# Kernel optimization log

Measured on AMD Instinct MI355X. Metric: run time of the kernel, lower is better.

## Reference

```python
import jax, jax.numpy as jnp
import numpy as np

B, L, HID = 4, 1024, 1024
H, D = 16, 64  # num heads, head size


def setup_inputs() -> dict:
    key = jax.random.key(0)
    ks = jax.random.split(key, 12)
    s = 0.02
    return {
        "hidden_states": jax.random.normal(ks[0], (B, L, HID), jnp.float32),
        "attention_mask": jnp.zeros((B, 1, 1, L), jnp.float32),
        "structure_matrix": jax.random.normal(ks[1], (L, L, D), jnp.float32),
        # torch nn.Linear weights are [out, in]
        "Wq": jax.random.normal(ks[2], (H * D, HID), jnp.float32) * s,
        "bq": jnp.zeros((H * D,), jnp.float32),
        "Wk": jax.random.normal(ks[3], (H * D, HID), jnp.float32) * s,
        "bk": jnp.zeros((H * D,), jnp.float32),
        "Wv": jax.random.normal(ks[4], (H * D, HID), jnp.float32) * s,
        "bv": jnp.zeros((H * D,), jnp.float32),
        "Wsq": jax.random.normal(ks[5], (D, D), jnp.float32) * s,
        "bsq": jnp.zeros((D,), jnp.float32),
        "Wsk": jax.random.normal(ks[6], (D, D), jnp.float32) * s,
        "bsk": jnp.zeros((D,), jnp.float32),
    }


def _heads(x):
    # [B, L, H*D] -> [B, H, L, D]
    return x.reshape(B, L, H, D).transpose(0, 2, 1, 3)


def reference(hidden_states, attention_mask, structure_matrix,
              Wq, bq, Wk, bk, Wv, bv, Wsq, bsq, Wsk, bsk):
    q = _heads(hidden_states @ Wq.T + bq)  # [B,H,L,D]
    k = _heads(hidden_states @ Wk.T + bk)
    v = _heads(hidden_states @ Wv.T + bv)

    scores = jnp.einsum('bhld,bhrd->bhlr', q, k)

    sq = structure_matrix @ Wsq.T + bsq  # [L,L,D]
    sk = structure_matrix @ Wsk.T + bsk
    scores = scores + jnp.einsum('bhld,lrd->bhlr', q, sq) \
                    + jnp.einsum('bhrd,lrd->bhlr', k, sk)

    scores = scores / jnp.sqrt(jnp.float32(D)) + attention_mask
    probs = jax.nn.softmax(scores, axis=-1)
    ctx = jnp.einsum('bhlr,bhrd->bhld', probs, v)
    ctx = ctx.transpose(0, 2, 1, 3).reshape(B, L, H * D)
    return ctx, scores
```

## Files before the change

kernel.cpp:

```cpp
#include <hip/hip_runtime.h>

typedef __attribute__((ext_vector_type(8))) short short8v;
typedef __attribute__((ext_vector_type(4))) short short4v;
typedef __attribute__((ext_vector_type(4))) float float4v;
typedef __attribute__((ext_vector_type(2))) unsigned int uint2v;

#define MFMA16(a,b,c) __builtin_amdgcn_mfma_f32_16x16x32_bf16(a,b,c,0,0,0)

__device__ __forceinline__ unsigned short f2b(float f) {
    union { float f; unsigned u; } v; v.f = f;
    unsigned r = v.u + 0x7FFFu + ((v.u >> 16) & 1u);
    return (unsigned short)(r >> 16);
}
__device__ __forceinline__ float b2f(unsigned short s) {
    union { unsigned u; float f; } v; v.u = ((unsigned)s) << 16;
    return v.f;
}
__device__ __forceinline__ short8v pack8(float4v a, float4v b) {
    union { unsigned u[4]; short8v s; } o;
    asm("v_cvt_pk_bf16_f32 %0, %1, %2" : "=v"(o.u[0]) : "v"(a[0]), "v"(a[1]));
    asm("v_cvt_pk_bf16_f32 %0, %1, %2" : "=v"(o.u[1]) : "v"(a[2]), "v"(a[3]));
    asm("v_cvt_pk_bf16_f32 %0, %1, %2" : "=v"(o.u[2]) : "v"(b[0]), "v"(b[1]));
    asm("v_cvt_pk_bf16_f32 %0, %1, %2" : "=v"(o.u[3]) : "v"(b[2]), "v"(b[3]));
    return o.s;
}

__global__ __launch_bounds__(256) void pack_all(
    const float* __restrict__ hidden, const float* __restrict__ Wq,
    const float* __restrict__ Wk, const float* __restrict__ Wv,
    unsigned short* __restrict__ hb, unsigned short* __restrict__ Wqb,
    unsigned short* __restrict__ Wkb, unsigned short* __restrict__ Wvb) {
    const int bid = blockIdx.x;
    const float* in; unsigned short* out; int i;
    if (bid < 2048)      { in = hidden; out = hb;  i = bid * 256 + threadIdx.x; }
    else if (bid < 2560) { in = Wq; out = Wqb; i = (bid - 2048) * 256 + threadIdx.x; }
    else if (bid < 3072) { in = Wk; out = Wkb; i = (bid - 2560) * 256 + threadIdx.x; }
    else                 { in = Wv; out = Wvb; i = (bid - 3072) * 256 + threadIdx.x; }
    float4v a = *(const float4v*)&in[(size_t)i * 8];
    float4v b = *(const float4v*)&in[(size_t)i * 8 + 4];
    *(short8v*)&out[(size_t)i * 8] = pack8(a, b);
}

__global__ __launch_bounds__(256) void qkv_gemm(
    const unsigned short* __restrict__ A,
    const unsigned short* __restrict__ W,
    const float* __restrict__ bias,
    unsigned short* __restrict__ out, int vmode) {
    const int wave = threadIdx.x >> 6, lane = threadIdx.x & 63;
    const int m0 = blockIdx.y * 128 + wave * 32;
    const int n0 = blockIdx.x * 64;
    const int lrow = lane & 15, g8 = (lane >> 4) << 3, row4 = (lane >> 4) << 2;
    float4v acc[2][4] = {};
    const unsigned short* Ap = A + (size_t)(m0 + lrow) * 1024 + g8;
    const unsigned short* Wp = W + (size_t)(n0 + lrow) * 1024 + g8;
#pragma unroll 2
    for (int k0 = 0; k0 < 1024; k0 += 32) {
        short8v a0 = *(const short8v*)(Ap + k0);
        short8v a1 = *(const short8v*)(Ap + 16 * 1024 + k0);
        short8v b0 = *(const short8v*)(Wp + k0);
        short8v b1 = *(const short8v*)(Wp + 16 * 1024 + k0);
        short8v b2 = *(const short8v*)(Wp + 32 * 1024 + k0);
        short8v b3 = *(const short8v*)(Wp + 48 * 1024 + k0);
        acc[0][0] = MFMA16(a0, b0, acc[0][0]); acc[0][1] = MFMA16(a0, b1, acc[0][1]);
        acc[0][2] = MFMA16(a0, b2, acc[0][2]); acc[0][3] = MFMA16(a0, b3, acc[0][3]);
        acc[1][0] = MFMA16(a1, b0, acc[1][0]); acc[1][1] = MFMA16(a1, b1, acc[1][1]);
        acc[1][2] = MFMA16(a1, b2, acc[1][2]); acc[1][3] = MFMA16(a1, b3, acc[1][3]);
    }
#pragma unroll
    for (int nt = 0; nt < 4; ++nt) {
        const int n = n0 + nt * 16 + lrow;
        const float bz = bias[n];
        const int h = n >> 6, d = n & 63;
#pragma unroll
        for (int mt = 0; mt < 2; ++mt) {
            const int mb = m0 + mt * 16 + row4;
            if (vmode == 0) {
#pragma unroll
                for (int j = 0; j < 4; ++j) {
                    const int m = mb + j;
                    const int b = m >> 10, l = m & 1023;
                    out[(((size_t)(b * 16 + h) << 10) + l) * 64 + d] = f2b(acc[mt][nt][j] + bz);
                }
            } else {
                const int b = mb >> 10, r = mb & 1023;
                short4v pk;
#pragma unroll
                for (int j = 0; j < 4; ++j) pk[j] = (short)f2b(acc[mt][nt][j] + bz);
                *(short4v*)&out[((((size_t)(b * 16 + h)) << 6) + d) * 1024 + r] = pk;
            }
        }
    }
}

__global__ __launch_bounds__(256) void headproj(
    const unsigned short* __restrict__ xh,
    const float* __restrict__ Wsx,
    const float* __restrict__ bsx,
    unsigned short* __restrict__ x2b,
    float* __restrict__ xbv) {
    __shared__ __align__(16) float Ws[64 * 64];
    __shared__ float bs[64];
    __shared__ __align__(16) unsigned short Xl[64 * 64];
    const int tid = threadIdx.x;
    const int l = blockIdx.x;
#pragma unroll
    for (int i = 0; i < 4; ++i)
        *(float4v*)&Ws[tid * 4 + i * 1024] = *(const float4v*)&Wsx[tid * 4 + i * 1024];
    if (tid < 64) bs[tid] = bsx[tid];
    {
        const int bhh = tid >> 2, dq = (tid & 3) * 16;
        const unsigned short* src = &xh[((size_t)bhh * 1024 + l) * 64 + dq];
        *(short8v*)&Xl[bhh * 64 + dq] = *(const short8v*)src;
        *(short8v*)&Xl[bhh * 64 + dq + 8] = *(const short8v*)(src + 8);
    }
    __syncthreads();
    const int bh = tid >> 2, e0 = (tid & 3) * 16;
    float acc[16] = {};
    float bacc = 0.f;
    for (int d = 0; d < 64; ++d) {
        const float xd = b2f(Xl[bh * 64 + d]);
        bacc += xd * bs[d];
        const float* wr = &Ws[d * 64 + e0];
#pragma unroll
        for (int e = 0; e < 16; e += 4) {
            float4v w = *(const float4v*)&wr[e];
            acc[e] += xd * w[0]; acc[e + 1] += xd * w[1];
            acc[e + 2] += xd * w[2]; acc[e + 3] += xd * w[3];
        }
    }
    short8v p0, p1;
#pragma unroll
    for (int e = 0; e < 8; ++e) { p0[e] = (short)f2b(acc[e]); p1[e] = (short)f2b(acc[e + 8]); }
    unsigned short* dst = &x2b[((size_t)l * 64 + bh) * 64 + e0];
    *(short8v*)dst = p0; *(short8v*)(dst + 8) = p1;
    if ((tid & 3) == 0) xbv[l * 64 + bh] = bacc;
}

__global__ __launch_bounds__(256, 4) void struct_fused(
    const float* __restrict__ S,
    const unsigned short* __restrict__ q2b,
    const unsigned short* __restrict__ k2b,
    const float* __restrict__ qbv,
    const float* __restrict__ kbv,
    unsigned short* __restrict__ sb) {
    __shared__ __align__(16) unsigned short Ssh[256 * 64];
    __shared__ __align__(16) unsigned short t3g[4][4][16][16];
    const int tid = threadIdx.x;
    const int w = tid >> 6, lane = tid & 63;
    const int lrow = lane & 15, g = lane >> 4;
    const int g8 = g << 3, row4 = g << 2;
    const int w16 = w << 4;
    const int r0 = blockIdx.x << 4, l0 = blockIdx.y << 4;

    {
        const int u = tid & 15, roff = tid >> 4;
        const float* gp = S + ((size_t)l0 * 1024 + r0 + roff) * 64 + u * 4;
        float4v f[16];
#pragma unroll
        for (int i = 0; i < 16; ++i)
            f[i] = *(const float4v*)(gp + (size_t)i * 65536);
#pragma unroll
        for (int i = 0; i < 16; ++i) {
            const int R = (i << 4) + roff;
            const int K3 = (roff ^ i) & 7;
            const int pu = u ^ (K3 << 1);
            union { unsigned uu[2]; uint2v v2; } o;
            asm("v_cvt_pk_bf16_f32 %0, %1, %2" : "=v"(o.uu[0]) : "v"(f[i][0]), "v"(f[i][1]));
            asm("v_cvt_pk_bf16_f32 %0, %1, %2" : "=v"(o.uu[1]) : "v"(f[i][2]), "v"(f[i][3]));
            *(uint2v*)&Ssh[(R << 6) + (pu << 2)] = o.v2;
        }
    }
    float kbreg[4];
#pragma unroll
    for (int j = 0; j < 4; ++j)
        kbreg[j] = kbv[(size_t)(r0 + row4 + j) * 64 + w16 + lrow];
    __syncthreads();

    float4v c3[16];
#pragma unroll
    for (int ri = 0; ri < 16; ++ri) {
        const int row = lrow * 16 + ri;
        const int key = (lrow ^ ri) & 7;
        short8v a0 = *(const short8v*)&Ssh[row * 64 + ((g ^ key) << 3)];
        short8v a1 = *(const short8v*)&Ssh[row * 64 + (((4 + g) ^ key) << 3)];
        const unsigned short* Bp = k2b + ((size_t)(r0 + ri) * 64 + w16 + lrow) * 64 + g8;
        short8v b0 = *(const short8v*)Bp;
        short8v b1 = *(const short8v*)(Bp + 32);
        float4v acc = {};
        acc = MFMA16(a0, b0, acc);
        acc = MFMA16(a1, b1, acc);
        c3[ri] = acc;
    }

#pragma unroll
    for (int G = 0; G < 4; ++G) {
        if (g == G) {
#pragma unroll
            for (int j = 0; j < 4; ++j) {
                float4v la{c3[0][j], c3[1][j], c3[2][j], c3[3][j]};
                float4v lb{c3[4][j], c3[5][j], c3[6][j], c3[7][j]};
                float4v ha{c3[8][j], c3[9][j], c3[10][j], c3[11][j]};
                float4v hb{c3[12][j], c3[13][j], c3[14][j], c3[15][j]};
                *(short8v*)&t3g[w][j][lrow][0] = pack8(la, lb);
                *(short8v*)&t3g[w][j][lrow][8] = pack8(ha, hb);
            }
        }
        asm volatile("s_waitcnt lgkmcnt(0)" ::: "memory");
#pragma unroll
        for (int lj = 0; lj < 4; ++lj) {
            const int li = (G << 2) + lj;
            const int row = li * 16 + lrow;
            const int key = (li ^ lrow) & 7;
            short8v a0 = *(const short8v*)&Ssh[row * 64 + ((g ^ key) << 3)];
            short8v a1 = *(const short8v*)&Ssh[row * 64 + (((4 + g) ^ key) << 3)];
            const unsigned short* Bp = q2b + ((size_t)(l0 + li) * 64 + w16 + lrow) * 64 + g8;
            short8v b0 = *(const short8v*)Bp;
            short8v b1 = *(const short8v*)(Bp + 32);
            float4v c2 = {};
            c2 = MFMA16(a0, b0, c2);
            c2 = MFMA16(a1, b1, c2);
            short4v t3v = *(const short4v*)&t3g[w][lj][lrow][row4];
            const float qb = qbv[(size_t)(l0 + li) * 64 + w16 + lrow];
            short4v outv;
#pragma unroll
            for (int j = 0; j < 4; ++j)
                outv[j] = (short)f2b(c2[j] + b2f((unsigned short)t3v[j]) + qb + kbreg[j]);
            *(short4v*)&sb[((size_t)(l0 + li) * 64 + w16 + lrow) * 1024 + r0 + row4] = outv;
        }
    }
}

__global__ __launch_bounds__(256) void flash_kernel(
    const unsigned short* __restrict__ qh,
    const unsigned short* __restrict__ kh,
    const unsigned short* __restrict__ vT,
    const unsigned short* __restrict__ sb,
    const float* __restrict__ mask,
    float* __restrict__ scores,
    float* __restrict__ ctx) {
    __shared__ __align__(16) float scL[32 * 64];
    __shared__ __align__(16) unsigned short pL[32 * 64];
    __shared__ float mL[32], sL[32], fL[32];
    const int bid = blockIdx.x;
    const int virt = (bid & 7) * 256 + (bid >> 3);
    const int bh = virt >> 5, lt = virt & 31;
    const int b = bh >> 4, h = bh & 15, l0 = lt * 32;
    const int tid = threadIdx.x, wave = tid >> 6, lane = tid & 63;
    const int lrow = lane & 15, g8 = (lane >> 4) << 3, row4 = (lane >> 4) << 2;
    short8v qf[2][2];
#pragma unroll
    for (int mt = 0; mt < 2; ++mt)
#pragma unroll
        for (int ks = 0; ks < 2; ++ks)
            qf[mt][ks] = *(const short8v*)&qh[((size_t)bh * 1024 + l0 + mt * 16 + lrow) * 64 + ks * 32 + g8];
    float4v opv[2] = {};
    if (tid < 32) { mL[tid] = -3e38f; sL[tid] = 0.f; }
    __syncthreads();
    const int tl = tid >> 3, tr8 = tid & 7;
    const int keyS = ((tl >> 2) & 3) << 4;
    const int keyP = (tl & 7) << 3;
    for (int rt = 0; rt < 16; ++rt) {
        const int r0 = rt * 64;
        float4v sacc[2] = {};
#pragma unroll
        for (int ks = 0; ks < 2; ++ks) {
            short8v kf = *(const short8v*)&kh[((size_t)bh * 1024 + r0 + wave * 16 + lrow) * 64 + ks * 32 + g8];
            sacc[0] = MFMA16(qf[0][ks], kf, sacc[0]);
            sacc[1] = MFMA16(qf[1][ks], kf, sacc[1]);
        }
#pragma unroll
        for (int mt = 0; mt < 2; ++mt)
#pragma unroll
            for (int j = 0; j < 4; ++j) {
                const int ll = mt * 16 + row4 + j;
                const int cc = wave * 16 + lrow;
                scL[ll * 64 + (cc ^ (((ll >> 2) & 3) << 4))] = sacc[mt][j];
            }
        __syncthreads();
        float4v x0 = *(const float4v*)&scL[tl * 64 + ((tr8 * 8) ^ keyS)];
        float4v x1 = *(const float4v*)&scL[tl * 64 + ((tr8 * 8 + 4) ^ keyS)];
        short8v sbv = *(const short8v*)&sb[((size_t)(l0 + tl) * 64 + bh) * 1024 + r0 + tr8 * 8];
        float4v mk0 = *(const float4v*)&mask[(size_t)b * 1024 + r0 + tr8 * 8];
        float4v mk1 = *(const float4v*)&mask[(size_t)b * 1024 + r0 + tr8 * 8 + 4];
        float s8[8];
#pragma unroll
        for (int i = 0; i < 4; ++i) {
            s8[i]     = (x0[i] + b2f((unsigned short)sbv[i])) * 0.125f + mk0[i];
            s8[i + 4] = (x1[i] + b2f((unsigned short)sbv[i + 4])) * 0.125f + mk1[i];
        }
        {
            float4v o0, o1;
#pragma unroll
            for (int i = 0; i < 4; ++i) { o0[i] = s8[i]; o1[i] = s8[i + 4]; }
            float* sgp = &scores[((size_t)bh * 1024 + l0 + tl) * 1024 + r0 + tr8 * 8];
            *(float4v*)sgp = o0; *(float4v*)(sgp + 4) = o1;
        }
        float tm = s8[0];
#pragma unroll
        for (int i = 1; i < 8; ++i) tm = fmaxf(tm, s8[i]);
        tm = fmaxf(tm, __shfl_xor(tm, 1));
        tm = fmaxf(tm, __shfl_xor(tm, 2));
        tm = fmaxf(tm, __shfl_xor(tm, 4));
        const float mold = mL[tl];
        const float mnew = fmaxf(mold, tm);
        const float f = __expf(mold - mnew);
        float psum = 0.f;
        float p8[8];
#pragma unroll
        for (int i = 0; i < 8; ++i) { p8[i] = __expf(s8[i] - mnew); psum += p8[i]; }
        psum += __shfl_xor(psum, 1);
        psum += __shfl_xor(psum, 2);
        psum += __shfl_xor(psum, 4);
        if (tr8 == 0) { sL[tl] = sL[tl] * f + psum; mL[tl] = mnew; fL[tl] = f; }
        short8v pk;
#pragma unroll
        for (int i = 0; i < 8; ++i) pk[i] = (short)f2b(p8[i]);
        *(short8v*)&pL[tl * 64 + ((tr8 * 8) ^ keyP)] = pk;
        __syncthreads();
#pragma unroll
        for (int mt = 0; mt < 2; ++mt)
#pragma unroll
            for (int j = 0; j < 4; ++j) opv[mt][j] *= fL[mt * 16 + row4 + j];
#pragma unroll
        for (int ks = 0; ks < 2; ++ks) {
            short8v pf0 = *(const short8v*)&pL[(lrow) * 64 + ((ks * 32 + g8) ^ ((lrow & 7) << 3))];
            short8v pf1 = *(const short8v*)&pL[(16 + lrow) * 64 + ((ks * 32 + g8) ^ ((lrow & 7) << 3))];
            short8v vf = *(const short8v*)&vT[((size_t)bh * 64 + wave * 16 + lrow) * 1024 + r0 + ks * 32 + g8];
            opv[0] = MFMA16(pf0, vf, opv[0]);
            opv[1] = MFMA16(pf1, vf, opv[1]);
        }
    }
#pragma unroll
    for (int mt = 0; mt < 2; ++mt)
#pragma unroll
        for (int j = 0; j < 4; ++j) {
            const int l = mt * 16 + row4 + j;
            const float inv = 1.f / sL[l];
            const int d = wave * 16 + lrow;
            ctx[((size_t)b * 1024 + l0 + l) * 1024 + h * 64 + d] = opv[mt][j] * inv;
        }
}

extern "C" void kernel_launch(void* const* d_in, const int* in_sizes, int n_in,
                              void* d_out, int out_size, void* d_ws, size_t ws_size,
                              hipStream_t stream) {
    (void)in_sizes; (void)n_in; (void)out_size; (void)ws_size;
    const float* hidden = (const float*)d_in[0];
    const float* mask   = (const float*)d_in[1];
    const float* S      = (const float*)d_in[2];
    const float* Wq  = (const float*)d_in[3];  const float* bq  = (const float*)d_in[4];
    const float* Wk  = (const float*)d_in[5];  const float* bk  = (const float*)d_in[6];
    const float* Wv  = (const float*)d_in[7];  const float* bv  = (const float*)d_in[8];
    const float* Wsq = (const float*)d_in[9];  const float* bsq = (const float*)d_in[10];
    const float* Wsk = (const float*)d_in[11]; const float* bsk = (const float*)d_in[12];

    float* ctx    = (float*)d_out;
    float* scores = ctx + (size_t)4 * 1024 * 1024;

    char* ws = (char*)d_ws;
    unsigned short* sbuf = (unsigned short*)ws;
    unsigned short* hb  = (unsigned short*)ws;
    unsigned short* Wqb = (unsigned short*)(ws + (8u << 20));
    unsigned short* Wkb = (unsigned short*)(ws + (10u << 20));
    unsigned short* Wvb = (unsigned short*)(ws + (12u << 20));
    unsigned short* qh  = (unsigned short*)(ws + (size_t)(128u) * 1024 * 1024);
    unsigned short* kh  = qh  + (size_t)4 * 1024 * 1024;
    unsigned short* vT  = kh  + (size_t)4 * 1024 * 1024;
    unsigned short* q2b = vT  + (size_t)4 * 1024 * 1024;
    unsigned short* k2b = q2b + (size_t)4 * 1024 * 1024;
    float* qbv = (float*)(k2b + (size_t)4 * 1024 * 1024);
    float* kbv = qbv + 65536;

    pack_all<<<3584, 256, 0, stream>>>(hidden, Wq, Wk, Wv, hb, Wqb, Wkb, Wvb);
    qkv_gemm<<<dim3(16, 32), 256, 0, stream>>>(hb, Wqb, bq, qh, 0);
    qkv_gemm<<<dim3(16, 32), 256, 0, stream>>>(hb, Wkb, bk, kh, 0);
    qkv_gemm<<<dim3(16, 32), 256, 0, stream>>>(hb, Wvb, bv, vT, 1);
    headproj<<<1024, 256, 0, stream>>>(qh, Wsq, bsq, q2b, qbv);
    headproj<<<1024, 256, 0, stream>>>(kh, Wsk, bsk, k2b, kbv);
    struct_fused<<<dim3(64, 64), 256, 0, stream>>>(S, q2b, k2b, qbv, kbv, sbuf);
    flash_kernel<<<2048, 256, 0, stream>>>(qh, kh, vT, sbuf, mask, scores, ctx);
}
```

Baseline: 541.7 us.

## Give each wave its own query rows in flash kernel and merge QKV GEMM launches

The flash kernel now assigns each wave an independent 32-row query tile, so a block covers 128 rows and the grid drops to 512 blocks. Each wave computes transposed score tiles (K as the A operand), keeps row max and sum in registers with cross-lane shuffles, and stages P in a per-wave double-buffered LDS slot. This removes the block-wide __syncthreads and the shared-memory score round trip. The three QKV GEMM launches are merged into one 48-column grid that picks Q, K or V weights by block index. In exchange, each wave reloads its own K and V tiles and holds more accumulator registers, and fewer blocks are launched.

```diff
diff --git a/kernel.cpp b/kernel.cpp
--- a/kernel.cpp
+++ b/kernel.cpp
@@ -43,12 +43,20 @@
 
 __global__ __launch_bounds__(256) void qkv_gemm(
     const unsigned short* __restrict__ A,
-    const unsigned short* __restrict__ W,
-    const float* __restrict__ bias,
-    unsigned short* __restrict__ out, int vmode) {
+    const unsigned short* __restrict__ Wqb, const unsigned short* __restrict__ Wkb,
+    const unsigned short* __restrict__ Wvb,
+    const float* __restrict__ bq, const float* __restrict__ bk,
+    const float* __restrict__ bv,
+    unsigned short* __restrict__ outq) {
+    const int n0g = blockIdx.x * 64;
+    const int which = n0g >> 10;
+    const int n0 = n0g & 1023;
+    const unsigned short* W = (which == 0) ? Wqb : (which == 1) ? Wkb : Wvb;
+    const float* bias = (which == 0) ? bq : (which == 1) ? bk : bv;
+    unsigned short* out = outq + (size_t)which * 4194304;
+    const int vmode = (which == 2);
     const int wave = threadIdx.x >> 6, lane = threadIdx.x & 63;
     const int m0 = blockIdx.y * 128 + wave * 32;
-    const int n0 = blockIdx.x * 64;
     const int lrow = lane & 15, g8 = (lane >> 4) << 3, row4 = (lane >> 4) << 2;
     float4v acc[2][4] = {};
     const unsigned short* Ap = A + (size_t)(m0 + lrow) * 1024 + g8;
@@ -238,107 +246,114 @@
     const float* __restrict__ mask,
     float* __restrict__ scores,
     float* __restrict__ ctx) {
-    __shared__ __align__(16) float scL[32 * 64];
-    __shared__ __align__(16) unsigned short pL[32 * 64];
-    __shared__ float mL[32], sL[32], fL[32];
+    __shared__ __align__(16) unsigned short pL[2][4][2][16][64];
     const int bid = blockIdx.x;
-    const int virt = (bid & 7) * 256 + (bid >> 3);
-    const int bh = virt >> 5, lt = virt & 31;
-    const int b = bh >> 4, h = bh & 15, l0 = lt * 32;
-    const int tid = threadIdx.x, wave = tid >> 6, lane = tid & 63;
-    const int lrow = lane & 15, g8 = (lane >> 4) << 3, row4 = (lane >> 4) << 2;
+    const int bh  = (bid & 7) * 8 + ((bid >> 3) & 7);
+    const int seg = bid >> 6;
+    const int tid = threadIdx.x, w = tid >> 6, lane = tid & 63;
+    const int l0 = ((seg << 2) | w) << 5;
+    const int b = bh >> 4, h = bh & 15;
+    const int lam = lane & 15, g = lane >> 4, g8 = g << 3, g4 = g << 2;
+    const int key = (lam & 7) << 1;
+
     short8v qf[2][2];
 #pragma unroll
     for (int mt = 0; mt < 2; ++mt)
 #pragma unroll
         for (int ks = 0; ks < 2; ++ks)
-            qf[mt][ks] = *(const short8v*)&qh[((size_t)bh * 1024 + l0 + mt * 16 + lrow) * 64 + ks * 32 + g8];
-    float4v opv[2] = {};
-    if (tid < 32) { mL[tid] = -3e38f; sL[tid] = 0.f; }
-    __syncthreads();
-    const int tl = tid >> 3, tr8 = tid & 7;
-    const int keyS = ((tl >> 2) & 3) << 4;
-    const int keyP = (tl & 7) << 3;
+            qf[mt][ks] = *(const short8v*)&qh[((size_t)bh * 1024 + l0 + mt * 16 + lam) * 64 + ks * 32 + g8];
+    const int myl[2] = { l0 + lam, l0 + 16 + lam };
+    float mrun[2] = { -3e38f, -3e38f }, sden[2] = { 0.f, 0.f };
+    float4v opv[2][4] = {};
+
     for (int rt = 0; rt < 16; ++rt) {
-        const int r0 = rt * 64;
-        float4v sacc[2] = {};
+        const int r0 = rt << 6;
+        const int pc = rt & 1;
+        float4v sacc[2][4] = {};
+#pragma unroll
+        for (int rs = 0; rs < 4; ++rs)
+#pragma unroll
+            for (int ks = 0; ks < 2; ++ks) {
+                short8v kf = *(const short8v*)&kh[((size_t)bh * 1024 + r0 + rs * 16 + lam) * 64 + ks * 32 + g8];
+                sacc[0][rs] = MFMA16(kf, qf[0][ks], sacc[0][rs]);
+                sacc[1][rs] = MFMA16(kf, qf[1][ks], sacc[1][rs]);
+            }
+        float s8[2][4][4];
+        float mx[2] = { -3e38f, -3e38f };
+#pragma unroll
+        for (int rs = 0; rs < 4; ++rs) {
+            float4v mk = *(const float4v*)&mask[(size_t)b * 1024 + r0 + rs * 16 + g4];
+#pragma unroll
+            for (int mt = 0; mt < 2; ++mt) {
+                short4v sbv = *(const short4v*)&sb[((size_t)myl[mt] * 64 + bh) * 1024 + r0 + rs * 16 + g4];
+                float4v o;
+#pragma unroll
+                for (int j = 0; j < 4; ++j) {
+                    const float v = (sacc[mt][rs][j] + b2f((unsigned short)sbv[j])) * 0.125f + mk[j];
+                    s8[mt][rs][j] = v; o[j] = v;
+                    mx[mt] = fmaxf(mx[mt], v);
+                }
+                *(float4v*)&scores[((size_t)bh * 1024 + myl[mt]) * 1024 + r0 + rs * 16 + g4] = o;
+            }
+        }
+#pragma unroll
+        for (int mt = 0; mt < 2; ++mt) {
+            float t = mx[mt];
+            t = fmaxf(t, __shfl_xor(t, 16));
+            t = fmaxf(t, __shfl_xor(t, 32));
+            const float mn = fmaxf(mrun[mt], t);
+            const float f = __expf(mrun[mt] - mn);
+            mrun[mt] = mn;
+            float ps = 0.f;
+#pragma unroll
+            for (int rs = 0; rs < 4; ++rs)
+#pragma unroll
+                for (int j = 0; j < 4; ++j) {
+                    const float p = __expf(s8[mt][rs][j] - mn);
+                    s8[mt][rs][j] = p; ps += p;
+                }
+            ps += __shfl_xor(ps, 16);
+            ps += __shfl_xor(ps, 32);
+            sden[mt] = sden[mt] * f + ps;
+#pragma unroll
+            for (int dt = 0; dt < 4; ++dt)
+#pragma unroll
+                for (int j = 0; j < 4; ++j) opv[mt][dt][j] *= f;
+        }
+#pragma unroll
+        for (int mt = 0; mt < 2; ++mt)
+#pragma unroll
+            for (int rs = 0; rs < 4; ++rs) {
+                union { unsigned uu[2]; uint2v v2; } o;
+                asm("v_cvt_pk_bf16_f32 %0, %1, %2" : "=v"(o.uu[0]) : "v"(s8[mt][rs][0]), "v"(s8[mt][rs][1]));
+                asm("v_cvt_pk_bf16_f32 %0, %1, %2" : "=v"(o.uu[1]) : "v"(s8[mt][rs][2]), "v"(s8[mt][rs][3]));
+                const int unit = ((rs << 2) | g) ^ key;
+                *(uint2v*)&pL[pc][w][mt][lam][unit << 2] = o.v2;
+            }
 #pragma unroll
         for (int ks = 0; ks < 2; ++ks) {
-            short8v kf = *(const short8v*)&kh[((size_t)bh * 1024 + r0 + wave * 16 + lrow) * 64 + ks * 32 + g8];
-            sacc[0] = MFMA16(qf[0][ks], kf, sacc[0]);
-            sacc[1] = MFMA16(qf[1][ks], kf, sacc[1]);
-        }
-#pragma unroll
-        for (int mt = 0; mt < 2; ++mt)
-#pragma unroll
-            for (int j = 0; j < 4; ++j) {
-                const int ll = mt * 16 + row4 + j;
-                const int cc = wave * 16 + lrow;
-                scL[ll * 64 + (cc ^ (((ll >> 2) & 3) << 4))] = sacc[mt][j];
-            }
-        __syncthreads();
-        float4v x0 = *(const float4v*)&scL[tl * 64 + ((tr8 * 8) ^ keyS)];
-        float4v x1 = *(const float4v*)&scL[tl * 64 + ((tr8 * 8 + 4) ^ keyS)];
-        short8v sbv = *(const short8v*)&sb[((size_t)(l0 + tl) * 64 + bh) * 1024 + r0 + tr8 * 8];
-        float4v mk0 = *(const float4v*)&mask[(size_t)b * 1024 + r0 + tr8 * 8];
-        float4v mk1 = *(const float4v*)&mask[(size_t)b * 1024 + r0 + tr8 * 8 + 4];
-        float s8[8];
-#pragma unroll
-        for (int i = 0; i < 4; ++i) {
-            s8[i]     = (x0[i] + b2f((unsigned short)sbv[i])) * 0.125f + mk0[i];
-            s8[i + 4] = (x1[i] + b2f((unsigned short)sbv[i + 4])) * 0.125f + mk1[i];
-        }
-        {
-            float4v o0, o1;
-#pragma unroll
-            for (int i = 0; i < 4; ++i) { o0[i] = s8[i]; o1[i] = s8[i + 4]; }
-            float* sgp = &scores[((size_t)bh * 1024 + l0 + tl) * 1024 + r0 + tr8 * 8];
-            *(float4v*)sgp = o0; *(float4v*)(sgp + 4) = o1;
-        }
-        float tm = s8[0];
-#pragma unroll
-        for (int i = 1; i < 8; ++i) tm = fmaxf(tm, s8[i]);
-        tm = fmaxf(tm, __shfl_xor(tm, 1));
-        tm = fmaxf(tm, __shfl_xor(tm, 2));
-        tm = fmaxf(tm, __shfl_xor(tm, 4));
-        const float mold = mL[tl];
-        const float mnew = fmaxf(mold, tm);
-        const float f = __expf(mold - mnew);
-        float psum = 0.f;
-        float p8[8];
-#pragma unroll
-        for (int i = 0; i < 8; ++i) { p8[i] = __expf(s8[i] - mnew); psum += p8[i]; }
-        psum += __shfl_xor(psum, 1);
-        psum += __shfl_xor(psum, 2);
-        psum += __shfl_xor(psum, 4);
-        if (tr8 == 0) { sL[tl] = sL[tl] * f + psum; mL[tl] = mnew; fL[tl] = f; }
-        short8v pk;
-#pragma unroll
-        for (int i = 0; i < 8; ++i) pk[i] = (short)f2b(p8[i]);
-        *(short8v*)&pL[tl * 64 + ((tr8 * 8) ^ keyP)] = pk;
-        __syncthreads();
-#pragma unroll
-        for (int mt = 0; mt < 2; ++mt)
-#pragma unroll
-            for (int j = 0; j < 4; ++j) opv[mt][j] *= fL[mt * 16 + row4 + j];
-#pragma unroll
-        for (int ks = 0; ks < 2; ++ks) {
-            short8v pf0 = *(const short8v*)&pL[(lrow) * 64 + ((ks * 32 + g8) ^ ((lrow & 7) << 3))];
-            short8v pf1 = *(const short8v*)&pL[(16 + lrow) * 64 + ((ks * 32 + g8) ^ ((lrow & 7) << 3))];
-            short8v vf = *(const short8v*)&vT[((size_t)bh * 64 + wave * 16 + lrow) * 1024 + r0 + ks * 32 + g8];
-            opv[0] = MFMA16(pf0, vf, opv[0]);
-            opv[1] = MFMA16(pf1, vf, opv[1]);
-        }
-    }
-#pragma unroll
-    for (int mt = 0; mt < 2; ++mt)
-#pragma unroll
-        for (int j = 0; j < 4; ++j) {
-            const int l = mt * 16 + row4 + j;
-            const float inv = 1.f / sL[l];
-            const int d = wave * 16 + lrow;
-            ctx[((size_t)b * 1024 + l0 + l) * 1024 + h * 64 + d] = opv[mt][j] * inv;
-        }
+            const int u = (((ks << 3) | (g << 1)) ^ key) << 2;
+            short8v pb0 = *(const short8v*)&pL[pc][w][0][lam][u];
+            short8v pb1 = *(const short8v*)&pL[pc][w][1][lam][u];
+#pragma unroll
+            for (int dt = 0; dt < 4; ++dt) {
+                short8v va = *(const short8v*)&vT[((size_t)bh * 64 + dt * 16 + lam) * 1024 + r0 + ks * 32 + g8];
+                opv[0][dt] = MFMA16(va, pb0, opv[0][dt]);
+                opv[1][dt] = MFMA16(va, pb1, opv[1][dt]);
+            }
+        }
+    }
+#pragma unroll
+    for (int mt = 0; mt < 2; ++mt) {
+        const float inv = 1.f / sden[mt];
+#pragma unroll
+        for (int dt = 0; dt < 4; ++dt) {
+            float4v o;
+#pragma unroll
+            for (int j = 0; j < 4; ++j) o[j] = opv[mt][dt][j] * inv;
+            *(float4v*)&ctx[((size_t)b * 1024 + myl[mt]) * 1024 + h * 64 + dt * 16 + g4] = o;
+        }
+    }
 }
 
 extern "C" void kernel_launch(void* const* d_in, const int* in_sizes, int n_in,
@@ -372,11 +387,9 @@
     float* kbv = qbv + 65536;
 
     pack_all<<<3584, 256, 0, stream>>>(hidden, Wq, Wk, Wv, hb, Wqb, Wkb, Wvb);
-    qkv_gemm<<<dim3(16, 32), 256, 0, stream>>>(hb, Wqb, bq, qh, 0);
-    qkv_gemm<<<dim3(16, 32), 256, 0, stream>>>(hb, Wkb, bk, kh, 0);
-    qkv_gemm<<<dim3(16, 32), 256, 0, stream>>>(hb, Wvb, bv, vT, 1);
+    qkv_gemm<<<dim3(48, 32), 256, 0, stream>>>(hb, Wqb, Wkb, Wvb, bq, bk, bv, qh);
     headproj<<<1024, 256, 0, stream>>>(qh, Wsq, bsq, q2b, qbv);
     headproj<<<1024, 256, 0, stream>>>(kh, Wsk, bsk, k2b, kbv);
     struct_fused<<<dim3(64, 64), 256, 0, stream>>>(S, q2b, k2b, qbv, kbv, sbuf);
-    flash_kernel<<<2048, 256, 0, stream>>>(qh, kh, vT, sbuf, mask, scores, ctx);
-}
+    flash_kernel<<<512, 256, 0, stream>>>(qh, kh, vT, sbuf, mask, scores, ctx);
+}
```

New measurement: 539.1 us. Within noise of the previous version (-0.5%).
